# Optimization experiments

Hardware: AMD Instinct MI355X
Metric: run time of the kernel (lower is better)

Reference implementation:

```python
import jax, jax.numpy as jnp
import numpy as np
from jax import lax

N = 4096
D = 256          # dim_hidden
DU = 1024        # dim_uni
G = 2000         # num_genes
E = 4            # num_experts
K = 1            # top-k
H = 4            # attention heads
HD = D // H      # head dim = 64
MAP = 64         # fourier mapping_size


def _ln(x, g, b, eps=1e-5):
    m = jnp.mean(x, axis=-1, keepdims=True)
    v = jnp.var(x, axis=-1, keepdims=True)
    return (x - m) * lax.rsqrt(v + eps) * g + b


def setup_inputs() -> dict:
    key = jax.random.key(0)
    ks = jax.random.split(key, 32)
    s = 0.02
    inp = {
        "vis": jax.random.normal(ks[0], (N, DU), jnp.float32),
        "pos": jax.random.uniform(ks[1], (N, 3), jnp.float32),
        "grad": jax.random.uniform(ks[2], (N, 1), jnp.float32),
        # FourierEncoding buffer: randn(3, 64) * scale(10)
        "B_fourier": jax.random.normal(ks[3], (3, MAP), jnp.float32) * 10.0,
        # img_enc
        "W_img": jax.random.normal(ks[4], (DU, D), jnp.float32) * s,
        "b_img": jnp.zeros((D,), jnp.float32),
        # pos_enc linear: Linear(128, 256)
        "W_pos": jax.random.normal(ks[5], (2 * MAP, D), jnp.float32) * s,
        "b_pos": jnp.zeros((D,), jnp.float32),
        # MultiheadAttention projections
        "Wq": jax.random.normal(ks[6], (D, D), jnp.float32) * s,
        "bq": jnp.zeros((D,), jnp.float32),
        "Wk": jax.random.normal(ks[7], (D, D), jnp.float32) * s,
        "bk": jnp.zeros((D,), jnp.float32),
        "Wv": jax.random.normal(ks[8], (D, D), jnp.float32) * s,
        "bv": jnp.zeros((D,), jnp.float32),
        "Wo": jax.random.normal(ks[9], (D, D), jnp.float32) * s,
        "bo": jnp.zeros((D,), jnp.float32),
        "ln1_g": jnp.ones((D,), jnp.float32),
        "ln1_b": jnp.zeros((D,), jnp.float32),
        # MoE router: Linear(D+1, E)
        "W_router": jax.random.normal(ks[10], (D + 1, E), jnp.float32) * s,
        "b_router": jnp.zeros((E,), jnp.float32),
        # experts: stacked [E, ...] FFN weights
        "W1e": jax.random.normal(ks[11], (E, D, 4 * D), jnp.float32) * s,
        "b1e": jnp.zeros((E, 4 * D), jnp.float32),
        "W2e": jax.random.normal(ks[12], (E, 4 * D, D), jnp.float32) * s,
        "b2e": jnp.zeros((E, D), jnp.float32),
        # gene decoder
        "Wg1": jax.random.normal(ks[13], (D, D), jnp.float32) * s,
        "bg1": jnp.zeros((D,), jnp.float32),
        "lng_g": jnp.ones((D,), jnp.float32),
        "lng_b": jnp.zeros((D,), jnp.float32),
        "Wg2": jax.random.normal(ks[14], (D, 2 * G), jnp.float32) * s,
        "bg2": jnp.zeros((2 * G,), jnp.float32),
        # func head
        "Wf1": jax.random.normal(ks[15], (D, 64), jnp.float32) * s,
        "bf1": jnp.zeros((64,), jnp.float32),
        "Wf2": jax.random.normal(ks[16], (64, 1), jnp.float32) * s,
        "bf2": jnp.zeros((1,), jnp.float32),
    }
    return inp


def reference(vis, pos, grad, B_fourier, W_img, b_img, W_pos, b_pos,
              Wq, bq, Wk, bk, Wv, bv, Wo, bo, ln1_g, ln1_b,
              W_router, b_router, W1e, b1e, W2e, b2e,
              Wg1, bg1, lng_g, lng_b, Wg2, bg2, Wf1, bf1, Wf2, bf2):
    # --- encoders ---
    x_proj = (2.0 * np.pi) * (pos @ B_fourier)                 # [N, 64]
    fourier = jnp.concatenate([jnp.sin(x_proj), jnp.cos(x_proj)], axis=-1)  # [N,128]
    z = vis @ W_img + b_img + fourier @ W_pos + b_pos          # [N, D]

    # --- spatial context attention (batch=1 full self-attention) ---
    q = (z @ Wq + bq).reshape(N, H, HD)
    k = (z @ Wk + bk).reshape(N, H, HD)
    v = (z @ Wv + bv).reshape(N, H, HD)
    scores = jnp.einsum('nhd,mhd->hnm', q, k) / np.sqrt(HD)    # [H, N, N]
    attn = jax.nn.softmax(scores, axis=-1)
    ctx = jnp.einsum('hnm,mhd->nhd', attn, v).reshape(N, D)
    attn_out = ctx @ Wo + bo
    z = _ln(z + attn_out, ln1_g, ln1_b)

    # --- sparse MoE (top-1 routing, gated dense expert combine) ---
    router_in = jnp.concatenate([z, grad], axis=-1)            # [N, D+1]
    logits = router_in @ W_router + b_router                   # [N, E]
    probs = jax.nn.softmax(logits, axis=-1)
    topk_p, topk_i = lax.top_k(probs, K)                       # [N, K]
    gate = jnp.sum(jax.nn.one_hot(topk_i, E, dtype=z.dtype) * topk_p[..., None], axis=1)  # [N, E]
    h = jax.nn.gelu(jnp.einsum('nd,edf->nef', z, W1e) + b1e, approximate=False)  # [N,E,4D]
    y = jnp.einsum('nef,efd->ned', h, W2e) + b2e               # [N, E, D]
    z = z + jnp.einsum('ne,ned->nd', gate, y)

    # --- gene decoder ---
    d = jax.nn.gelu(_ln(z @ Wg1 + bg1, lng_g, lng_b), approximate=False)
    preds = (d @ Wg2 + bg2).reshape(N, G, 2)
    mu = jax.nn.softplus(preds[:, :, 0])
    theta = jax.nn.softplus(preds[:, :, 1]) + 1e-6

    # --- functional head ---
    g = jax.nn.sigmoid(jax.nn.gelu(z @ Wf1 + bf1, approximate=False) @ Wf2 + bf2)
    return mu, theta, g
```

## Files before the change

### kernel.cpp

```cpp
#include <hip/hip_runtime.h>
#include <math.h>

#define NTOK 4096
#define DMODEL 256
#define G_GENES 2000

typedef _Float16 f16;
typedef _Float16 f16x2 __attribute__((ext_vector_type(2)));
typedef _Float16 f16x8 __attribute__((ext_vector_type(8)));
typedef float f32x4 __attribute__((ext_vector_type(4)));

__device__ __forceinline__ float gelu_exact(float x) {
    return 0.5f * x * (1.0f + erff(x * 0.70710678118654752f));
}
__device__ __forceinline__ float softplus_fast(float x) {
    return fmaxf(x, 0.0f) + __logf(1.0f + __expf(-fabsf(x)));
}
__device__ __forceinline__ unsigned pkf16(float a, float b) {
    union { f16x2 h; unsigned u; } t;
    t.h = (f16x2){(f16)a, (f16)b};
    return t.u;
}

__global__ __launch_bounds__(256) void encin_k(const float* __restrict__ vis,
                                               const float* __restrict__ pos,
                                               const float* __restrict__ B,
                                               f16* __restrict__ Abig) {
    int n = blockIdx.x, t = threadIdx.x;
    float4 v = *(const float4*)(vis + (size_t)n * 1024 + t * 4);
    union { ushort4 u; f16 h[4]; } o;
    o.h[0] = (f16)v.x; o.h[1] = (f16)v.y; o.h[2] = (f16)v.z; o.h[3] = (f16)v.w;
    *(ushort4*)(Abig + (size_t)n * 1152 + t * 4) = o.u;
    if (t < 64) {
        float xp = 6.283185307179586f *
                   (pos[n * 3 + 0] * B[t] + pos[n * 3 + 1] * B[64 + t] + pos[n * 3 + 2] * B[128 + t]);
        Abig[(size_t)n * 1152 + 1024 + t] = (f16)sinf(xp);
        Abig[(size_t)n * 1152 + 1088 + t] = (f16)cosf(xp);
    }
}

struct TD { const float* s; f16* d; int R, C; int ldo; };
struct TDs { TD t[17]; int pre[18]; };
__global__ __launch_bounds__(256) void tconv_k(TDs ds) {
    int bid = blockIdx.x;
    int ti = 0;
#pragma unroll
    for (int i = 0; i < 17; i++)
        if (bid >= ds.pre[i + 1]) ti = i + 1;
    TD td = ds.t[ti];
    int local = bid - ds.pre[ti];
    int yt = td.C >> 5;
    int r0 = (local / yt) << 5;
    int c0 = (local % yt) << 5;
    __shared__ float tile[32][33];
    int tx = threadIdx.x & 31, ty = threadIdx.x >> 5;
#pragma unroll
    for (int i = 0; i < 32; i += 8)
        tile[ty + i][tx] = td.s[(size_t)(r0 + ty + i) * td.C + c0 + tx];
    __syncthreads();
#pragma unroll
    for (int i = 0; i < 32; i += 8)
        td.d[(size_t)(c0 + ty + i) * td.ldo + r0 + tx] = (f16)tile[tx][ty + i];
}

__global__ __launch_bounds__(256) void tconvh_k(const f16* __restrict__ src, int ldin,
                                                f16* __restrict__ dst, int ldo) {
    __shared__ f16 tile[32][33];
    int r0 = blockIdx.x * 32, c0 = blockIdx.y * 32;
    int tx = threadIdx.x & 31, ty = threadIdx.x >> 5;
#pragma unroll
    for (int i = 0; i < 32; i += 8)
        tile[ty + i][tx] = src[(size_t)(r0 + ty + i) * ldin + c0 + tx];
    __syncthreads();
#pragma unroll
    for (int i = 0; i < 32; i += 8)
        dst[(size_t)(c0 + ty + i) * ldo + r0 + tx] = tile[tx][ty + i];
}

__global__ __launch_bounds__(256) void setup_k(const float* b_img, const float* b_pos,
                                               const float* bq, const float* bk, const float* bv,
                                               const float* bg1, const float* bf1,
                                               float* benc, float* biasqkv, float* bgf) {
    int t = threadIdx.x;
    benc[t] = b_img[t] + b_pos[t];
    biasqkv[t] = bq[t];
    biasqkv[256 + t] = bk[t];
    biasqkv[512 + t] = bv[t];
    bgf[t] = bg1[t];
    if (t < 64) bgf[256 + t] = bf1[t];
}

#define EPI_F32 0
#define EPI_DUAL 1
#define EPI_F16 2
#define EPI_GELU_F16 3
#define EPI_GENE 4
#define EPI_MOESC 5
#define EPI_GF 6

template <int MTN, int EPI, int MODE>
__global__ __launch_bounds__(256) void bgemm_k(
    const f16* __restrict__ A, int lda,
    const f16* __restrict__ B, int ldb,
    const float* __restrict__ bias,
    float* __restrict__ Cf, f16* __restrict__ Ch, int ldc,
    int Ncols, int K,
    size_t eB, size_t eBias,
    const int* __restrict__ gidx, const int* __restrict__ temap,
    const float* __restrict__ z2, const float* __restrict__ gval,
    float* __restrict__ outMu, float* __restrict__ outTheta) {
    constexpr int BN = MTN * 32;
    __shared__ __align__(16) char smem[(128 + BN) * 72 * 2];
    f16 (*As)[72] = (f16(*)[72])smem;
    f16 (*Bs)[72] = (f16(*)[72])(smem + (size_t)128 * 72 * 2);

    const int tid = threadIdx.x;
    const int m0 = blockIdx.x * 128;
    const int n0 = blockIdx.y * BN;
    const int w = tid >> 6, lane = tid & 63;
    const int wr = w >> 1, wc = w & 1;
    const int ln = lane & 15, lg = lane >> 4;
    const int sr = tid >> 3;
    const int sc = (tid & 7) * 8;

    if (MODE == 1 || MODE == 2) {
        int e = temap[blockIdx.x];
        B += (size_t)e * eB;
        if (bias) bias += (size_t)e * eBias;
    }

    int grows[4];
#pragma unroll
    for (int i = 0; i < 4; i++) {
        int r = m0 + sr + i * 32;
        if (MODE == 1) {
            int g = gidx[r];
            grows[i] = (g < 0) ? 0 : g;
        } else {
            grows[i] = r;
        }
    }

    f32x4 acc[4][MTN];
    f32x4 zf = {0.f, 0.f, 0.f, 0.f};
#pragma unroll
    for (int i = 0; i < 4; i++)
#pragma unroll
        for (int j = 0; j < MTN; j++) acc[i][j] = zf;

    for (int k0 = 0; k0 < K; k0 += 64) {
#pragma unroll
        for (int i = 0; i < 4; i++) {
            uint4 v = *(const uint4*)(A + (size_t)grows[i] * lda + k0 + sc);
            int r = sr + i * 32;
            *(uint2*)&As[r][sc] = make_uint2(v.x, v.y);
            *(uint2*)&As[r][sc + 4] = make_uint2(v.z, v.w);
        }
#pragma unroll
        for (int i = 0; i < MTN; i++) {
            int r = sr + i * 32;
            uint4 v = make_uint4(0, 0, 0, 0);
            if (n0 + r < Ncols) v = *(const uint4*)(B + (size_t)(n0 + r) * ldb + k0 + sc);
            *(uint2*)&Bs[r][sc] = make_uint2(v.x, v.y);
            *(uint2*)&Bs[r][sc + 4] = make_uint2(v.z, v.w);
        }
        __syncthreads();
#pragma unroll
        for (int ks = 0; ks < 64; ks += 32) {
            f16x8 a[4], b[MTN];
#pragma unroll
            for (int t = 0; t < 4; t++) {
                const f16* p = &As[wr * 64 + t * 16 + ln][ks + lg * 8];
                union { f16x8 f; uint2 u[2]; } tmp;
                tmp.u[0] = *(const uint2*)p;
                tmp.u[1] = *(const uint2*)(p + 4);
                a[t] = tmp.f;
            }
#pragma unroll
            for (int t = 0; t < MTN; t++) {
                const f16* p = &Bs[wc * (MTN * 16) + t * 16 + ln][ks + lg * 8];
                union { f16x8 f; uint2 u[2]; } tmp;
                tmp.u[0] = *(const uint2*)p;
                tmp.u[1] = *(const uint2*)(p + 4);
                b[t] = tmp.f;
            }
#pragma unroll
            for (int tm = 0; tm < 4; tm++)
#pragma unroll
                for (int tn = 0; tn < MTN; tn++)
                    acc[tm][tn] = __builtin_amdgcn_mfma_f32_16x16x32_f16(a[tm], b[tn], acc[tm][tn], 0, 0, 0);
        }
        __syncthreads();
    }

    if (EPI == EPI_GENE) {
        float bval[MTN];
#pragma unroll
        for (int tn = 0; tn < MTN; tn++) {
            int col = n0 + wc * (MTN * 16) + tn * 16 + ln;
            bval[tn] = (col < Ncols) ? bias[col] : 0.0f;
        }
        float* Cs = (float*)smem;
        const int rrow = tid >> 3;
        const int rseg = tid & 7;
#pragma unroll
        for (int tm = 0; tm < 4; tm++) {
            __syncthreads();
#pragma unroll
            for (int tn = 0; tn < MTN; tn++) {
                int lc = wc * (MTN * 16) + tn * 16 + ln;
#pragma unroll
                for (int i = 0; i < 4; i++) {
                    int lr = wr * 16 + lg * 4 + i;
                    Cs[lr * 132 + lc] = acc[tm][tn][i] + bval[tn];
                }
            }
            __syncthreads();
            int grow = m0 + ((rrow >> 4) * 64) + tm * 16 + (rrow & 15);
            const float* cr = &Cs[rrow * 132 + rseg * 16];
            float mu[8], th[8];
#pragma unroll
            for (int g = 0; g < 8; g++) {
                mu[g] = softplus_fast(cr[2 * g]);
                th[g] = softplus_fast(cr[2 * g + 1]) + 1e-6f;
            }
            int gbase = (n0 + rseg * 16) >> 1;
            float* mp = outMu + (size_t)grow * G_GENES + gbase;
            float* tp = outTheta + (size_t)grow * G_GENES + gbase;
            if (gbase + 8 <= G_GENES) {
                *(float4*)mp = make_float4(mu[0], mu[1], mu[2], mu[3]);
                *(float4*)(mp + 4) = make_float4(mu[4], mu[5], mu[6], mu[7]);
                *(float4*)tp = make_float4(th[0], th[1], th[2], th[3]);
                *(float4*)(tp + 4) = make_float4(th[4], th[5], th[6], th[7]);
            } else {
#pragma unroll
                for (int g = 0; g < 8; g++)
                    if (gbase + g < G_GENES) { mp[g] = mu[g]; tp[g] = th[g]; }
            }
        }
        return;
    }

#pragma unroll
    for (int tm = 0; tm < 4; tm++) {
#pragma unroll
        for (int tn = 0; tn < MTN; tn++) {
            int col = n0 + wc * (MTN * 16) + tn * 16 + ln;
            if (col >= Ncols) continue;
#pragma unroll
            for (int i = 0; i < 4; i++) {
                int row = m0 + wr * 64 + tm * 16 + lg * 4 + i;
                float v = acc[tm][tn][i];
                if (EPI == EPI_MOESC) {
                    int tok = gidx[row];
                    if (tok < 0) continue;
                    v += bias[col];
                    size_t oi = (size_t)tok * ldc + col;
                    Ch[oi] = (f16)(z2[oi] + gval[tok] * v);
                    continue;
                }
                if (EPI == EPI_GF) {
                    v += bias[col];
                    if (col < 256) Cf[(size_t)row * 256 + col] = v;
                    else Ch[(size_t)row * 64 + (col - 256)] = (f16)gelu_exact(v);
                    continue;
                }
                size_t idx = (size_t)row * ldc + col;
                if (EPI == EPI_F32) {
                    if (bias) v += bias[col];
                    Cf[idx] = v;
                } else if (EPI == EPI_DUAL) {
                    v += bias[col];
                    Cf[idx] = v;
                    Ch[idx] = (f16)v;
                } else if (EPI == EPI_F16) {
                    v += bias[col];
                    Ch[idx] = (f16)v;
                } else if (EPI == EPI_GELU_F16) {
                    v += bias[col];
                    Ch[idx] = (f16)gelu_exact(v);
                }
            }
        }
    }
}

__global__ __launch_bounds__(256) void flash_k(const f16* __restrict__ qkv,
                                               const f16* __restrict__ Vt,
                                               f16* __restrict__ Opart16,
                                               float2* __restrict__ mlpart) {
    __shared__ f16 Kb[2][64][72];
    __shared__ f16 Vb[2][64][72];
    const int tid = threadIdx.x;
    const int w = tid >> 6, lane = tid & 63;
    const int ln = lane & 15, quad = lane >> 4;
    const int q0 = blockIdx.x * 64;
    const int hq = blockIdx.y * 64;
    const int kt0 = blockIdx.z * 16;

    f16x8 qfrag[2];
    {
        const f16* qp = qkv + (size_t)(q0 + w * 16 + ln) * 768 + hq + quad * 8;
        union { f16x8 f; uint4 u; } t0, t1;
        t0.u = *(const uint4*)qp;
        t1.u = *(const uint4*)(qp + 32);
        qfrag[0] = t0.f; qfrag[1] = t1.f;
    }

    const int srow = tid >> 2;
    const int scol = (tid & 3) * 16;

    float m_run = -1e30f, l_run = 0.0f;
    f32x4 accO[4];
#pragma unroll
    for (int i = 0; i < 4; i++) accO[i] = (f32x4){0.f, 0.f, 0.f, 0.f};

    uint4 kA[2], vA[2], kB[2], vB[2];
    auto loadKV = [&](int kt, uint4* kr, uint4* vr) {
        const f16* kp = qkv + (size_t)(kt * 64 + srow) * 768 + 256 + hq + scol;
        const f16* vp = Vt + (size_t)(hq + srow) * 4096 + kt * 64 + scol;
        kr[0] = *(const uint4*)kp; kr[1] = *(const uint4*)(kp + 8);
        vr[0] = *(const uint4*)vp; vr[1] = *(const uint4*)(vp + 8);
    };
    auto stage = [&](int b, const uint4* kr, const uint4* vr) {
        *(uint4*)&Kb[b][srow][scol] = kr[0];
        *(uint4*)&Kb[b][srow][scol + 8] = kr[1];
        *(uint4*)&Vb[b][srow][scol] = vr[0];
        *(uint4*)&Vb[b][srow][scol + 8] = vr[1];
    };

    auto computeTile = [&](int b) {
        f32x4 accS[4];
#pragma unroll
        for (int nt = 0; nt < 4; nt++) {
            union { f16x8 f; uint4 u; } a0, a1;
            a0.u = *(const uint4*)&Kb[b][nt * 16 + ln][quad * 8];
            a1.u = *(const uint4*)&Kb[b][nt * 16 + ln][32 + quad * 8];
            f32x4 a = {0.f, 0.f, 0.f, 0.f};
            a = __builtin_amdgcn_mfma_f32_16x16x32_f16(a0.f, qfrag[0], a, 0, 0, 0);
            a = __builtin_amdgcn_mfma_f32_16x16x32_f16(a1.f, qfrag[1], a, 0, 0, 0);
            accS[nt] = a;
        }
        float mx = -1e30f;
#pragma unroll
        for (int nt = 0; nt < 4; nt++)
#pragma unroll
            for (int i = 0; i < 4; i++) {
                accS[nt][i] *= 0.125f;
                mx = fmaxf(mx, accS[nt][i]);
            }
        mx = fmaxf(mx, __shfl_xor(mx, 16));
        mx = fmaxf(mx, __shfl_xor(mx, 32));
        float mnew = fmaxf(m_run, mx);
        float rs = 0.0f;
#pragma unroll
        for (int nt = 0; nt < 4; nt++)
#pragma unroll
            for (int i = 0; i < 4; i++) {
                float p = __expf(accS[nt][i] - mnew);
                accS[nt][i] = p;
                rs += p;
            }
        rs += __shfl_xor(rs, 16);
        rs += __shfl_xor(rs, 32);
        float alpha = __expf(m_run - mnew);
        l_run = l_run * alpha + rs;
        m_run = mnew;
#pragma unroll
        for (int dt = 0; dt < 4; dt++)
#pragma unroll
            for (int i = 0; i < 4; i++) accO[dt][i] *= alpha;

#pragma unroll
        for (int c = 0; c < 2; c++) {
            unsigned p0x = pkf16(accS[2 * c][0], accS[2 * c][1]);
            unsigned p0y = pkf16(accS[2 * c][2], accS[2 * c][3]);
            unsigned p1x = pkf16(accS[2 * c + 1][0], accS[2 * c + 1][1]);
            unsigned p1y = pkf16(accS[2 * c + 1][2], accS[2 * c + 1][3]);
            unsigned x16_0x = __shfl_xor((int)p0x, 16), x16_0y = __shfl_xor((int)p0y, 16);
            unsigned x32_0x = __shfl_xor((int)p0x, 32), x32_0y = __shfl_xor((int)p0y, 32);
            unsigned x48_0x = __shfl_xor((int)p0x, 48), x48_0y = __shfl_xor((int)p0y, 48);
            unsigned x16_1x = __shfl_xor((int)p1x, 16), x16_1y = __shfl_xor((int)p1y, 16);
            unsigned x32_1x = __shfl_xor((int)p1x, 32), x32_1y = __shfl_xor((int)p1y, 32);
            unsigned x48_1x = __shfl_xor((int)p1x, 48), x48_1y = __shfl_xor((int)p1y, 48);
            union { f16x8 f; unsigned u[4]; } pf;
            pf.u[0] = quad == 0 ? p0x : quad == 1 ? x48_0x : quad == 2 ? x32_1x : x16_1x;
            pf.u[1] = quad == 0 ? p0y : quad == 1 ? x48_0y : quad == 2 ? x32_1y : x16_1y;
            pf.u[2] = quad == 0 ? x16_0x : quad == 1 ? x32_0x : quad == 2 ? x48_1x : p1x;
            pf.u[3] = quad == 0 ? x16_0y : quad == 1 ? x32_0y : quad == 2 ? x48_1y : p1y;
#pragma unroll
            for (int dt = 0; dt < 4; dt++) {
                union { f16x8 f; uint4 u; } vf;
                vf.u = *(const uint4*)&Vb[b][dt * 16 + ln][c * 32 + quad * 8];
                accO[dt] = __builtin_amdgcn_mfma_f32_16x16x32_f16(vf.f, pf.f, accO[dt], 0, 0, 0);
            }
        }
    };

    loadKV(kt0, kA, vA);
    stage(0, kA, vA);
    loadKV(kt0 + 1, kB, vB);
    __syncthreads();
    for (int t = 0; t < 16; t += 2) {
        computeTile(0);
        stage(1, kB, vB);
        if (t + 2 < 16) loadKV(kt0 + t + 2, kA, vA);
        __syncthreads();
        computeTile(1);
        if (t + 2 < 16) stage(0, kA, vA);
        if (t + 3 < 16) loadKV(kt0 + t + 3, kB, vB);
        __syncthreads();
    }

    const int slot = blockIdx.x * 4 + blockIdx.y;
    f16* op = Opart16 + ((((size_t)blockIdx.z * 256 + slot) * 4 + w) * 64 + lane) * 16;
    union { uint4 u; f16 h[8]; } pk0, pk1;
#pragma unroll
    for (int dt = 0; dt < 2; dt++)
#pragma unroll
        for (int i = 0; i < 4; i++) pk0.h[dt * 4 + i] = (f16)accO[dt][i];
#pragma unroll
    for (int dt = 2; dt < 4; dt++)
#pragma unroll
        for (int i = 0; i < 4; i++) pk1.h[(dt - 2) * 4 + i] = (f16)accO[dt][i];
    *(uint4*)op = pk0.u;
    *(uint4*)(op + 8) = pk1.u;
    if (quad == 0)
        mlpart[(size_t)(blockIdx.z * 4 + blockIdx.y) * NTOK + q0 + w * 16 + ln] =
            make_float2(m_run, l_run);
}

__global__ __launch_bounds__(256) void fcomb_k(const f16* __restrict__ Opart16,
                                               const float2* __restrict__ mlpart,
                                               f16* __restrict__ ctxbf) {
    __shared__ f16 Os[4][16][72];
    const int slot = blockIdx.x;
    const int w = threadIdx.x >> 6, lane = threadIdx.x & 63;
    const int bx = slot >> 2, h = slot & 3;
    const int quad = lane >> 4, ln = lane & 15;
    const int q = bx * 64 + w * 16 + ln;

    float2 ml[4];
    float mmax = -1e30f;
#pragma unroll
    for (int s = 0; s < 4; s++) {
        ml[s] = mlpart[(size_t)(s * 4 + h) * NTOK + q];
        mmax = fmaxf(mmax, ml[s].x);
    }
    float L = 0.0f, wgt[4];
#pragma unroll
    for (int s = 0; s < 4; s++) {
        wgt[s] = __expf(ml[s].x - mmax);
        L += wgt[s] * ml[s].y;
    }
    float acc[16];
#pragma unroll
    for (int j = 0; j < 16; j++) acc[j] = 0.f;
#pragma unroll
    for (int s = 0; s < 4; s++) {
        const f16* op = Opart16 + ((((size_t)s * 256 + slot) * 4 + w) * 64 + lane) * 16;
        union { uint4 u; f16 hh[8]; } p0, p1;
        p0.u = *(const uint4*)op;
        p1.u = *(const uint4*)(op + 8);
#pragma unroll
        for (int j = 0; j < 8; j++) {
            acc[j] += wgt[s] * (float)p0.hh[j];
            acc[8 + j] += wgt[s] * (float)p1.hh[j];
        }
    }
    float inv = 1.0f / L;
#pragma unroll
    for (int dt = 0; dt < 4; dt++)
#pragma unroll
        for (int i = 0; i < 4; i++)
            Os[w][ln][dt * 16 + quad * 4 + i] = (f16)(acc[dt * 4 + i] * inv);
    union { uint4 u; f16 hh[8]; } o0, o1;
    o0.u = *(const uint4*)&Os[w][ln][quad * 16];
    o1.u = *(const uint4*)&Os[w][ln][quad * 16 + 8];
    f16* cp = ctxbf + (size_t)q * 256 + h * 64 + quad * 16;
    *(uint4*)cp = o0.u;
    *(uint4*)(cp + 8) = o1.u;
}

template <int DO_ROUTER>
__global__ __launch_bounds__(256) void ln_k(const float* __restrict__ X,
                                            const float* __restrict__ R,
                                            const float* __restrict__ gam,
                                            const float* __restrict__ bet,
                                            float* __restrict__ Of, f16* __restrict__ Oh, int doGelu,
                                            const float* __restrict__ grad,
                                            const float* __restrict__ Wr,
                                            const float* __restrict__ br,
                                            int* __restrict__ eid, float* __restrict__ gval) {
    __shared__ float sm[4];
    __shared__ float smr[16];
    int n = blockIdx.x, c = threadIdx.x;
    float x = X[(size_t)n * DMODEL + c];
    if (R) x += R[(size_t)n * DMODEL + c];
    float s = x;
    for (int off = 32; off; off >>= 1) s += __shfl_down(s, off);
    if ((c & 63) == 0) sm[c >> 6] = s;
    __syncthreads();
    float mean = (sm[0] + sm[1] + sm[2] + sm[3]) * (1.0f / DMODEL);
    float d = x - mean;
    float s2 = d * d;
    for (int off = 32; off; off >>= 1) s2 += __shfl_down(s2, off);
    __syncthreads();
    if ((c & 63) == 0) sm[c >> 6] = s2;
    __syncthreads();
    float var = (sm[0] + sm[1] + sm[2] + sm[3]) * (1.0f / DMODEL);
    float y = d * rsqrtf(var + 1e-5f) * gam[c] + bet[c];
    if (doGelu) y = gelu_exact(y);
    size_t idx = (size_t)n * DMODEL + c;
    if (Of) Of[idx] = y;
    if (Oh) Oh[idx] = (f16)y;

    if (DO_ROUTER) {
        float p0 = y * Wr[c * 4 + 0], p1 = y * Wr[c * 4 + 1];
        float p2 = y * Wr[c * 4 + 2], p3 = y * Wr[c * 4 + 3];
        for (int off = 32; off; off >>= 1) {
            p0 += __shfl_down(p0, off);
            p1 += __shfl_down(p1, off);
            p2 += __shfl_down(p2, off);
            p3 += __shfl_down(p3, off);
        }
        int wv = c >> 6;
        if ((c & 63) == 0) {
            smr[wv * 4 + 0] = p0; smr[wv * 4 + 1] = p1;
            smr[wv * 4 + 2] = p2; smr[wv * 4 + 3] = p3;
        }
        __syncthreads();
        if (c == 0) {
            float gv = grad[n];
            float l[4];
#pragma unroll
            for (int e = 0; e < 4; e++)
                l[e] = smr[e] + smr[4 + e] + smr[8 + e] + smr[12 + e] + gv * Wr[256 * 4 + e] + br[e];
            float mx = fmaxf(fmaxf(l[0], l[1]), fmaxf(l[2], l[3]));
            float ex[4], ssum = 0;
#pragma unroll
            for (int e = 0; e < 4; e++) { ex[e] = __expf(l[e] - mx); ssum += ex[e]; }
            int am = 0;
            float best = l[0];
#pragma unroll
            for (int e = 1; e < 4; e++)
                if (l[e] > best) { best = l[e]; am = e; }
            eid[n] = am;
            gval[n] = ex[am] / ssum;
        }
    }
}

__global__ __launch_bounds__(256) void compact_k(const int* __restrict__ eid,
                                                 int* __restrict__ gidx,
                                                 int* __restrict__ temap) {
    __shared__ int cnt[4], poff[4], cur[4];
    int t = threadIdx.x;
    if (t < 4) cnt[t] = 0;
    __syncthreads();
    for (int it = 0; it < 16; it++)
        atomicAdd(&cnt[eid[it * 256 + t]], 1);
    __syncthreads();
    if (t == 0) {
        int o = 0;
        for (int e = 0; e < 4; e++) {
            poff[e] = o;
            cur[e] = o;
            o += (cnt[e] + 127) & ~127;
        }
    }
    __syncthreads();
    if (t < 36) {
        int e = 0;
        for (int x = 0; x < 4; x++) {
            int seg0 = poff[x] >> 7;
            int seg1 = (poff[x] + ((cnt[x] + 127) & ~127)) >> 7;
            if (t >= seg0 && t < seg1) e = x;
        }
        temap[t] = e;
    }
    for (int i = t; i < 4608; i += 256) gidx[i] = -1;
    __syncthreads();
    for (int it = 0; it < 16; it++) {
        int n = it * 256 + t;
        int slot = atomicAdd(&cur[eid[n]], 1);
        gidx[slot] = n;
    }
}

__global__ __launch_bounds__(256) void ghead_k(const f16* __restrict__ f,
                                               const float* __restrict__ Wf2,
                                               const float* __restrict__ bf2,
                                               float* __restrict__ out) {
    int n = blockIdx.x * 256 + threadIdx.x;
    float s = bf2[0];
#pragma unroll
    for (int c = 0; c < 8; c++) {
        union { uint4 u; f16 h[8]; } t;
        t.u = *(const uint4*)(f + (size_t)n * 64 + c * 8);
#pragma unroll
        for (int j = 0; j < 8; j++) s = fmaf((float)t.h[j], Wf2[c * 8 + j], s);
    }
    out[n] = 1.0f / (1.0f + expf(-s));
}

extern "C" void kernel_launch(void* const* d_in, const int* in_sizes, int n_in,
                              void* d_out, int out_size, void* d_ws, size_t ws_size,
                              hipStream_t stream) {
    const float* vis   = (const float*)d_in[0];
    const float* pos   = (const float*)d_in[1];
    const float* grad  = (const float*)d_in[2];
    const float* Bf    = (const float*)d_in[3];
    const float* W_img = (const float*)d_in[4];
    const float* b_img = (const float*)d_in[5];
    const float* W_pos = (const float*)d_in[6];
    const float* b_pos = (const float*)d_in[7];
    const float* Wq = (const float*)d_in[8];  const float* bq = (const float*)d_in[9];
    const float* Wk = (const float*)d_in[10]; const float* bk = (const float*)d_in[11];
    const float* Wv = (const float*)d_in[12]; const float* bv = (const float*)d_in[13];
    const float* Wo = (const float*)d_in[14]; const float* bo = (const float*)d_in[15];
    const float* ln1g = (const float*)d_in[16]; const float* ln1b = (const float*)d_in[17];
    const float* Wr = (const float*)d_in[18]; const float* br = (const float*)d_in[19];
    const float* W1e = (const float*)d_in[20]; const float* b1e = (const float*)d_in[21];
    const float* W2e = (const float*)d_in[22]; const float* b2e = (const float*)d_in[23];
    const float* Wg1 = (const float*)d_in[24]; const float* bg1 = (const float*)d_in[25];
    const float* lngg = (const float*)d_in[26]; const float* lngb = (const float*)d_in[27];
    const float* Wg2 = (const float*)d_in[28]; const float* bg2 = (const float*)d_in[29];
    const float* Wf1 = (const float*)d_in[30]; const float* bf1 = (const float*)d_in[31];
    const float* Wf2 = (const float*)d_in[32]; const float* bf2 = (const float*)d_in[33];

    float* out = (float*)d_out;
    float* outMu = out;
    float* outTh = out + (size_t)NTOK * G_GENES;
    float* outG  = out + (size_t)2 * NTOK * G_GENES;

    char* base = (char*)d_ws;
    size_t off = 0;
    auto A8 = [&](size_t bytes) { char* p = base + off; off += (bytes + 255) & ~(size_t)255; return p; };

    char* reg1 = A8(16 * 1024 * 1024);
    f16* Abig    = (f16*)reg1;
    f16* Opart16 = (f16*)reg1;
    char* reg2 = A8(20 * 1024 * 1024);
    f16* qkvbf = (f16*)reg2;
    f16* hh    = (f16*)(reg2 + 8 * 1024 * 1024);

    f16* WtEnc = (f16*)A8((size_t)256 * 1152 * 2);
    f16* Wqkvt = (f16*)A8((size_t)768 * 256 * 2);
    f16* Wot   = (f16*)A8((size_t)256 * 256 * 2);
    f16* W1t   = (f16*)A8((size_t)4 * 1024 * 256 * 2);
    f16* W2t   = (f16*)A8((size_t)4 * 256 * 1024 * 2);
    f16* Wgft  = (f16*)A8((size_t)320 * 256 * 2);
    f16* Wg2t  = (f16*)A8((size_t)4000 * 256 * 2);
    f16* Vt    = (f16*)A8((size_t)256 * NTOK * 2);
    float2* mlpart = (float2*)A8((size_t)16 * NTOK * 8);
    float* benc    = (float*)A8(256 * 4);
    float* biasqkv = (float*)A8(768 * 4);
    float* bgf     = (float*)A8(320 * 4);
    float* z    = (float*)A8((size_t)NTOK * DMODEL * 4);
    float* z2   = (float*)A8((size_t)NTOK * DMODEL * 4);
    float* attn = (float*)A8((size_t)NTOK * DMODEL * 4);
    float* tbuf = (float*)A8((size_t)NTOK * DMODEL * 4);
    f16* zbf    = (f16*)A8((size_t)NTOK * DMODEL * 2);
    f16* z2bf   = (f16*)A8((size_t)NTOK * DMODEL * 2);
    f16* z3bf   = (f16*)A8((size_t)NTOK * DMODEL * 2);
    f16* ctxbf  = (f16*)A8((size_t)NTOK * DMODEL * 2);
    f16* dbufbf = (f16*)A8((size_t)NTOK * DMODEL * 2);
    f16* fbf    = (f16*)A8((size_t)NTOK * 64 * 2);
    int* eidb   = (int*)A8(NTOK * 4);
    float* gval = (float*)A8(NTOK * 4);
    int* gidx   = (int*)A8(4608 * 4);
    int* temap  = (int*)A8(64 * 4);

    dim3 blk(256);

    TDs td;
    int nd = 0, pre = 0;
    auto addT = [&](const float* s, f16* d, int R, int C, int ldo) {
        td.t[nd] = TD{s, d, R, C, ldo};
        td.pre[nd] = pre;
        pre += (R >> 5) * (C >> 5);
        nd++;
    };
    addT(W_img, WtEnc, 1024, 256, 1152);
    addT(W_pos, WtEnc + 1024, 128, 256, 1152);
    addT(Wq, Wqkvt, 256, 256, 256);
    addT(Wk, Wqkvt + 256 * 256, 256, 256, 256);
    addT(Wv, Wqkvt + 512 * 256, 256, 256, 256);
    addT(Wo, Wot, 256, 256, 256);
    for (int e = 0; e < 4; e++) addT(W1e + (size_t)e * 262144, W1t + (size_t)e * 262144, 256, 1024, 256);
    for (int e = 0; e < 4; e++) addT(W2e + (size_t)e * 262144, W2t + (size_t)e * 262144, 1024, 256, 1024);
    addT(Wg1, Wgft, 256, 256, 256);
    addT(Wf1, Wgft + 256 * 256, 256, 64, 256);
    addT(Wg2, Wg2t, 256, 4000, 256);
    td.pre[nd] = pre;
    tconv_k<<<pre, blk, 0, stream>>>(td);
    setup_k<<<1, blk, 0, stream>>>(b_img, b_pos, bq, bk, bv, bg1, bf1, benc, biasqkv, bgf);

    encin_k<<<NTOK, blk, 0, stream>>>(vis, pos, Bf, Abig);
    bgemm_k<1, EPI_DUAL, 0><<<dim3(32, 8, 1), blk, 0, stream>>>(
        Abig, 1152, WtEnc, 1152, benc, z, zbf, 256, 256, 1152,
        0, 0, nullptr, nullptr, nullptr, nullptr, nullptr, nullptr);

    bgemm_k<2, EPI_F16, 0><<<dim3(32, 12, 1), blk, 0, stream>>>(
        zbf, 256, Wqkvt, 256, biasqkv, nullptr, qkvbf, 768, 768, 256,
        0, 0, nullptr, nullptr, nullptr, nullptr, nullptr, nullptr);
    tconvh_k<<<dim3(128, 8, 1), blk, 0, stream>>>(qkvbf + 512, 768, Vt, 4096);

    flash_k<<<dim3(64, 4, 4), blk, 0, stream>>>(qkvbf, Vt, Opart16, mlpart);
    fcomb_k<<<256, blk, 0, stream>>>(Opart16, mlpart, ctxbf);
    bgemm_k<1, EPI_F32, 0><<<dim3(32, 8, 1), blk, 0, stream>>>(
        ctxbf, 256, Wot, 256, bo, attn, nullptr, 256, 256, 256,
        0, 0, nullptr, nullptr, nullptr, nullptr, nullptr, nullptr);
    ln_k<1><<<NTOK, blk, 0, stream>>>(z, attn, ln1g, ln1b, z2, z2bf, 0, grad, Wr, br, eidb, gval);

    compact_k<<<1, blk, 0, stream>>>(eidb, gidx, temap);
    bgemm_k<4, EPI_GELU_F16, 1><<<dim3(36, 8, 1), blk, 0, stream>>>(
        z2bf, 256, W1t, 256, b1e, nullptr, hh, 1024, 1024, 256,
        262144, 1024, gidx, temap, nullptr, nullptr, nullptr, nullptr);
    bgemm_k<1, EPI_MOESC, 2><<<dim3(36, 8, 1), blk, 0, stream>>>(
        hh, 1024, W2t, 1024, b2e, nullptr, z3bf, 256, 256, 1024,
        262144, 256, gidx, temap, z2, gval, nullptr, nullptr);

    bgemm_k<1, EPI_GF, 0><<<dim3(32, 10, 1), blk, 0, stream>>>(
        z3bf, 256, Wgft, 256, bgf, tbuf, fbf, 256, 320, 256,
        0, 0, nullptr, nullptr, nullptr, nullptr, nullptr, nullptr);
    ln_k<0><<<NTOK, blk, 0, stream>>>(tbuf, nullptr, lngg, lngb, nullptr, dbufbf, 1,
                                      nullptr, nullptr, nullptr, nullptr, nullptr);
    bgemm_k<4, EPI_GENE, 0><<<dim3(32, 32, 1), blk, 0, stream>>>(
        dbufbf, 256, Wg2t, 256, bg2, nullptr, nullptr, 4000, 4000, 256,
        0, 0, nullptr, nullptr, nullptr, nullptr, outMu, outTh);

    ghead_k<<<NTOK / 256, blk, 0, stream>>>(fbf, Wf2, bf2, outG);
}
```

Before: 437.1 us.

## Split flash attention KV range eight ways with single-buffered LDS tiles

Doubles the KV split in the flash attention kernel from 4 to 8 chunks, so each block walks 8 key tiles instead of 16 and the grid doubles to 2048 blocks. The LDS double buffer becomes a single buffer with extra barriers around each stage, and launch bounds now request 6 blocks per CU, with the aim of raising occupancy and parallelism. The combine kernel now merges 8 partial results, and the m/l partial buffer is enlarged to match. Costs are more partial-output traffic, more combine work and more barrier stalls per tile. The Opart16 region must now hold twice the partial outputs.

New measurement: 449.5 us. 1.03x slower.

```diff
diff --git a/kernel.cpp b/kernel.cpp
--- a/kernel.cpp
+++ b/kernel.cpp
@@ -285,18 +285,18 @@
     }
 }
 
-__global__ __launch_bounds__(256) void flash_k(const f16* __restrict__ qkv,
-                                               const f16* __restrict__ Vt,
-                                               f16* __restrict__ Opart16,
-                                               float2* __restrict__ mlpart) {
-    __shared__ f16 Kb[2][64][72];
-    __shared__ f16 Vb[2][64][72];
+__global__ __launch_bounds__(256, 6) void flash_k(const f16* __restrict__ qkv,
+                                                  const f16* __restrict__ Vt,
+                                                  f16* __restrict__ Opart16,
+                                                  float2* __restrict__ mlpart) {
+    __shared__ f16 Kb[64][72];
+    __shared__ f16 Vb[64][72];
     const int tid = threadIdx.x;
     const int w = tid >> 6, lane = tid & 63;
     const int ln = lane & 15, quad = lane >> 4;
     const int q0 = blockIdx.x * 64;
     const int hq = blockIdx.y * 64;
-    const int kt0 = blockIdx.z * 16;
+    const int kt0 = blockIdx.z * 8;
 
     f16x8 qfrag[2];
     {
@@ -322,20 +322,20 @@
         kr[0] = *(const uint4*)kp; kr[1] = *(const uint4*)(kp + 8);
         vr[0] = *(const uint4*)vp; vr[1] = *(const uint4*)(vp + 8);
     };
-    auto stage = [&](int b, const uint4* kr, const uint4* vr) {
-        *(uint4*)&Kb[b][srow][scol] = kr[0];
-        *(uint4*)&Kb[b][srow][scol + 8] = kr[1];
-        *(uint4*)&Vb[b][srow][scol] = vr[0];
-        *(uint4*)&Vb[b][srow][scol + 8] = vr[1];
+    auto stage = [&](const uint4* kr, const uint4* vr) {
+        *(uint4*)&Kb[srow][scol] = kr[0];
+        *(uint4*)&Kb[srow][scol + 8] = kr[1];
+        *(uint4*)&Vb[srow][scol] = vr[0];
+        *(uint4*)&Vb[srow][scol + 8] = vr[1];
     };
 
-    auto computeTile = [&](int b) {
+    auto computeTile = [&]() {
         f32x4 accS[4];
 #pragma unroll
         for (int nt = 0; nt < 4; nt++) {
             union { f16x8 f; uint4 u; } a0, a1;
-            a0.u = *(const uint4*)&Kb[b][nt * 16 + ln][quad * 8];
-            a1.u = *(const uint4*)&Kb[b][nt * 16 + ln][32 + quad * 8];
+            a0.u = *(const uint4*)&Kb[nt * 16 + ln][quad * 8];
+            a1.u = *(const uint4*)&Kb[nt * 16 + ln][32 + quad * 8];
             f32x4 a = {0.f, 0.f, 0.f, 0.f};
             a = __builtin_amdgcn_mfma_f32_16x16x32_f16(a0.f, qfrag[0], a, 0, 0, 0);
             a = __builtin_amdgcn_mfma_f32_16x16x32_f16(a1.f, qfrag[1], a, 0, 0, 0);
@@ -391,25 +391,26 @@
 #pragma unroll
             for (int dt = 0; dt < 4; dt++) {
                 union { f16x8 f; uint4 u; } vf;
-                vf.u = *(const uint4*)&Vb[b][dt * 16 + ln][c * 32 + quad * 8];
+                vf.u = *(const uint4*)&Vb[dt * 16 + ln][c * 32 + quad * 8];
                 accO[dt] = __builtin_amdgcn_mfma_f32_16x16x32_f16(vf.f, pf.f, accO[dt], 0, 0, 0);
             }
         }
     };
 
     loadKV(kt0, kA, vA);
-    stage(0, kA, vA);
     loadKV(kt0 + 1, kB, vB);
-    __syncthreads();
-    for (int t = 0; t < 16; t += 2) {
-        computeTile(0);
-        stage(1, kB, vB);
-        if (t + 2 < 16) loadKV(kt0 + t + 2, kA, vA);
+#pragma unroll 1
+    for (int t = 0; t < 8; t += 2) {
         __syncthreads();
-        computeTile(1);
-        if (t + 2 < 16) stage(0, kA, vA);
-        if (t + 3 < 16) loadKV(kt0 + t + 3, kB, vB);
+        stage(kA, vA);
         __syncthreads();
+        if (t + 2 < 8) loadKV(kt0 + t + 2, kA, vA);
+        computeTile();
+        __syncthreads();
+        stage(kB, vB);
+        __syncthreads();
+        if (t + 3 < 8) loadKV(kt0 + t + 3, kB, vB);
+        computeTile();
     }
 
     const int slot = blockIdx.x * 4 + blockIdx.y;
@@ -440,16 +441,16 @@
     const int quad = lane >> 4, ln = lane & 15;
     const int q = bx * 64 + w * 16 + ln;
 
-    float2 ml[4];
+    float2 ml[8];
     float mmax = -1e30f;
 #pragma unroll
-    for (int s = 0; s < 4; s++) {
+    for (int s = 0; s < 8; s++) {
         ml[s] = mlpart[(size_t)(s * 4 + h) * NTOK + q];
         mmax = fmaxf(mmax, ml[s].x);
     }
-    float L = 0.0f, wgt[4];
-#pragma unroll
-    for (int s = 0; s < 4; s++) {
+    float L = 0.0f, wgt[8];
+#pragma unroll
+    for (int s = 0; s < 8; s++) {
         wgt[s] = __expf(ml[s].x - mmax);
         L += wgt[s] * ml[s].y;
     }
@@ -457,7 +458,7 @@
 #pragma unroll
     for (int j = 0; j < 16; j++) acc[j] = 0.f;
 #pragma unroll
-    for (int s = 0; s < 4; s++) {
+    for (int s = 0; s < 8; s++) {
         const f16* op = Opart16 + ((((size_t)s * 256 + slot) * 4 + w) * 64 + lane) * 16;
         union { uint4 u; f16 hh[8]; } p0, p1;
         p0.u = *(const uint4*)op;
@@ -653,7 +654,7 @@
     f16* Wgft  = (f16*)A8((size_t)320 * 256 * 2);
     f16* Wg2t  = (f16*)A8((size_t)4000 * 256 * 2);
     f16* Vt    = (f16*)A8((size_t)256 * NTOK * 2);
-    float2* mlpart = (float2*)A8((size_t)16 * NTOK * 8);
+    float2* mlpart = (float2*)A8((size_t)32 * NTOK * 8);
     float* benc    = (float*)A8(256 * 4);
     float* biasqkv = (float*)A8(768 * 4);
     float* bgf     = (float*)A8(320 * 4);
@@ -707,7 +708,7 @@
         0, 0, nullptr, nullptr, nullptr, nullptr, nullptr, nullptr);
     tconvh_k<<<dim3(128, 8, 1), blk, 0, stream>>>(qkvbf + 512, 768, Vt, 4096);
 
-    flash_k<<<dim3(64, 4, 4), blk, 0, stream>>>(qkvbf, Vt, Opart16, mlpart);
+    flash_k<<<dim3(64, 4, 8), blk, 0, stream>>>(qkvbf, Vt, Opart16, mlpart);
     fcomb_k<<<256, blk, 0, stream>>>(Opart16, mlpart, ctxbf);
     bgemm_k<1, EPI_F32, 0><<<dim3(32, 8, 1), blk, 0, stream>>>(
         ctxbf, 256, Wot, 256, bo, attn, nullptr, 256, 256, 256,
```
